# Kernel tuning notes

Measured on AMD Instinct MI355X. Metric: run time of the kernel, lower is better.

Reference implementation:

```python
import jax, jax.numpy as jnp
import numpy as np
from jax import lax

STRIDE = 16
ANCHOR_BASE = 16
PRE_NMS = 6000
POST_NMS = 2000
NMS_THRESH = 0.7


def _generate_anchors(base_size=16, ratios=(0.5, 1.0, 2.0), scales=(8, 16, 32)):
    w = h = float(base_size)
    x_ctr = 0.5 * (w - 1)
    y_ctr = 0.5 * (h - 1)
    size = w * h
    anchors = []
    for r in ratios:
        ws = np.round(np.sqrt(size / r))
        hs = np.round(ws * r)
        for s in scales:
            wss, hss = ws * s, hs * s
            anchors.append([x_ctr - 0.5 * (wss - 1), y_ctr - 0.5 * (hss - 1),
                            x_ctr + 0.5 * (wss - 1), y_ctr + 0.5 * (hss - 1)])
    return np.array(anchors, dtype=np.float32)  # [9,4]


def _all_anchors(width, height, stride):
    base = _generate_anchors(ANCHOR_BASE)  # [A,4]
    sx = np.arange(width, dtype=np.float32) * stride
    gy, gx = np.meshgrid(np.arange(height, dtype=np.float32) * stride, sx, indexing='ij')
    shifts = np.stack([gx.ravel(), gy.ravel(), gx.ravel(), gy.ravel()], axis=1)  # [K,4] h-major
    return jnp.asarray((shifts[:, None, :] + base[None, :, :]).reshape(-1, 4))  # [K*A,4]


def setup_inputs() -> dict:
    key = jax.random.key(0)
    k1, k2 = jax.random.split(key)
    H = W = 64
    bbox_deltas = jax.random.normal(k1, (1, 36, H, W), dtype=jnp.float32)
    scores = jax.random.uniform(k2, (1, 2, 9 * H, W), dtype=jnp.float32)
    return {"bbox_deltas": bbox_deltas, "scores": scores, "im_w": 1024, "im_h": 1024}


def reference(bbox_deltas, scores, im_w, im_h):
    H, W = bbox_deltas.shape[2], bbox_deltas.shape[3]
    # fg scores: reshape [1,2,9H,W] -> [1,18,H,W], take channels 9:18
    sc = scores.reshape(1, 18, H, W)[:, 9:, :, :].transpose(0, 2, 3, 1).reshape(-1)
    dl = bbox_deltas.transpose(0, 2, 3, 1).reshape(-1, 4)
    anchors = _all_anchors(W, H, STRIDE)

    # bbox_transform_inv (decode)
    aw = anchors[:, 2] - anchors[:, 0] + 1.0
    ah = anchors[:, 3] - anchors[:, 1] + 1.0
    acx = anchors[:, 0] + 0.5 * aw
    acy = anchors[:, 1] + 0.5 * ah
    pcx = dl[:, 0] * aw + acx
    pcy = dl[:, 1] * ah + acy
    pw = jnp.exp(dl[:, 2]) * aw
    ph = jnp.exp(dl[:, 3]) * ah
    x1 = jnp.clip(pcx - 0.5 * pw, 0.0, im_w - 1.0)
    y1 = jnp.clip(pcy - 0.5 * ph, 0.0, im_h - 1.0)
    x2 = jnp.clip(pcx + 0.5 * pw, 0.0, im_w - 1.0)
    y2 = jnp.clip(pcy + 0.5 * ph, 0.0, im_h - 1.0)
    props = jnp.stack([x1, y1, x2, y2], axis=1)

    # min-size filter
    thresh = 16.0 * (float(im_h) / float(im_w))
    keep_f = ((x2 - x1 + 1.0) >= thresh) & ((y2 - y1 + 1.0) >= thresh)
    sc_m = jnp.where(keep_f, sc, -jnp.inf)

    # pre-NMS top-k by score
    top_sc, idx = lax.top_k(sc_m, PRE_NMS)
    top_p = props[idx]  # [PRE_NMS,4], sorted by score desc
    valid = jnp.isfinite(top_sc)

    # pairwise IoU (with +1 box convention, as in py_cpu_nms)
    bx1, by1, bx2, by2 = top_p[:, 0], top_p[:, 1], top_p[:, 2], top_p[:, 3]
    areas = (bx2 - bx1 + 1.0) * (by2 - by1 + 1.0)
    iw = jnp.maximum(jnp.minimum(bx2[:, None], bx2[None, :]) - jnp.maximum(bx1[:, None], bx1[None, :]) + 1.0, 0.0)
    ih = jnp.maximum(jnp.minimum(by2[:, None], by2[None, :]) - jnp.maximum(by1[:, None], by1[None, :]) + 1.0, 0.0)
    inter = iw * ih
    iou = inter / (areas[:, None] + areas[None, :] - inter)
    sup = iou > NMS_THRESH  # [N,N]

    ar = jnp.arange(PRE_NMS)

    def body(i, keep):
        row = sup[i] & keep[i] & (ar > i)
        return keep & (~row)

    keep = lax.fori_loop(0, PRE_NMS, body, valid)

    # take first POST_NMS kept (in score order), scatter into fixed-size output
    rank = jnp.cumsum(keep.astype(jnp.int32)) - 1
    sel = keep & (rank < POST_NMS)
    dst = jnp.where(sel, rank, POST_NMS)  # invalid rows dumped into slot POST_NMS
    out_b = jnp.zeros((POST_NMS + 1, 4), dtype=jnp.float32).at[dst].set(
        jnp.where(sel[:, None], top_p, 0.0))[:POST_NMS]
    out_s = jnp.zeros((POST_NMS + 1,), dtype=jnp.float32).at[dst].set(
        jnp.where(sel, top_sc, 0.0))[:POST_NMS]
    blob = jnp.concatenate([jnp.zeros((POST_NMS, 1), dtype=jnp.float32), out_b], axis=1)
    return blob, out_s[:, None]
```

## Files before the change

kernel.cpp:

```cpp
#include <hip/hip_runtime.h>
#include <math.h>

typedef unsigned int u32;
typedef unsigned long long u64;

#define NANCH   36864
#define PRE     6000
#define POST    2000
#define NWORDS  94

#define OFF_PROPS   ((size_t)0)
#define OFF_SV      ((size_t)589824)
#define OFF_SORTED  ((size_t)884736)
#define OFF_SEL     ((size_t)932864)
#define OFF_MASK    ((size_t)1227776)
#define OFF_CTRL    ((size_t)5739776)
#define OFF_H1      ((size_t)5740032)
#define OFF_INVALW  ((size_t)5744384)
#define OFF_KEEPW   ((size_t)5745152)
#define ZERO_BYTES  ((size_t)(256 + 4352 + 768))

__device__ __constant__ float BA[9][4] = {
  {-84.f,-40.f,99.f,55.f},   {-176.f,-88.f,191.f,103.f}, {-360.f,-184.f,375.f,199.f},
  {-56.f,-56.f,71.f,71.f},   {-120.f,-120.f,135.f,135.f},{-248.f,-248.f,263.f,263.f},
  {-36.f,-80.f,51.f,95.f},   {-80.f,-168.f,95.f,183.f},  {-168.f,-344.f,183.f,359.f}};

__device__ __forceinline__ u32 key_bin(u32 key) {
  if (key < 0xBF000000u) return 0u;
  u32 b = ((key >> 13) - 0x5F800u) + 1u;
  return b > 1024u ? 1024u : b;
}

__global__ void decode_k(const float* __restrict__ deltas, const float* __restrict__ scores,
                         const int* __restrict__ imw_p, const int* __restrict__ imh_p,
                         float4* __restrict__ props, u64* __restrict__ sortvals,
                         u32* __restrict__ h1) {
  #pragma clang fp contract(off)
  int i = blockIdx.x * 256 + threadIdx.x;
  if (i >= NANCH) return;
  int a = i % 9;
  int pix = i / 9;
  int x = pix & 63, y = pix >> 6;

  float sc = scores[(9 + a) * 4096 + pix];
  float d0 = deltas[(a * 4 + 0) * 4096 + pix];
  float d1 = deltas[(a * 4 + 1) * 4096 + pix];
  float d2 = deltas[(a * 4 + 2) * 4096 + pix];
  float d3 = deltas[(a * 4 + 3) * 4096 + pix];

  float gx = (float)(x * 16), gy = (float)(y * 16);
  float ax1 = gx + BA[a][0], ay1 = gy + BA[a][1];
  float ax2 = gx + BA[a][2], ay2 = gy + BA[a][3];
  float aw = ax2 - ax1 + 1.0f, ah = ay2 - ay1 + 1.0f;
  float acx = ax1 + 0.5f * aw, acy = ay1 + 0.5f * ah;

  float pcx = d0 * aw + acx;
  float pcy = d1 * ah + acy;
  float pw = (float)exp((double)d2) * aw;
  float ph = (float)exp((double)d3) * ah;

  float imw1 = (float)imw_p[0] - 1.0f, imh1 = (float)imh_p[0] - 1.0f;
  float x1 = fminf(fmaxf(pcx - 0.5f * pw, 0.0f), imw1);
  float y1 = fminf(fmaxf(pcy - 0.5f * ph, 0.0f), imh1);
  float x2 = fminf(fmaxf(pcx + 0.5f * pw, 0.0f), imw1);
  float y2 = fminf(fmaxf(pcy + 0.5f * ph, 0.0f), imh1);
  props[i] = make_float4(x1, y1, x2, y2);

  float thresh = 16.0f * ((float)imh_p[0] / (float)imw_p[0]);
  bool keep = (x2 - x1 + 1.0f >= thresh) && (y2 - y1 + 1.0f >= thresh);
  u32 key = keep ? (__float_as_uint(sc) | 0x80000000u) : 0u;
  sortvals[i] = ((u64)key << 32) | (u64)(0xFFFFFFFFu - (u32)i);
  u32 bin = key_bin(key);
  if (bin) atomicAdd(&h1[bin], 1u);
}

__global__ void scan_k(const u32* __restrict__ h1, u32* __restrict__ ctrl) {
  int l = threadIdx.x;
  u32 loc[16], suf[16];
  #pragma unroll
  for (int k = 0; k < 16; ++k) loc[k] = h1[1 + l * 16 + k];
  u32 acc = 0;
  #pragma unroll
  for (int k = 15; k >= 0; --k) { acc += loc[k]; suf[k] = acc; }
  u32 sfx = acc;
  for (int off = 1; off < 64; off <<= 1) {
    u32 o = __shfl_down(sfx, off);
    if (l + off < 64) sfx += o;
  }
  u32 S_above = sfx - acc;
  u64 mball = __ballot(suf[0] + S_above >= (u32)PRE);
  if (mball == 0ULL) { if (l == 0) ctrl[0] = 0u; return; }
  int L = 63 - __builtin_clzll(mball);
  if (l == L) {
    int kk = 0;
    for (int k = 15; k >= 0; --k)
      if (suf[k] + S_above >= (u32)PRE) { kk = k; break; }
    ctrl[0] = (u32)(1 + 16 * L + kk);
  }
}

__global__ void compact_k(const u64* __restrict__ sv, u32* __restrict__ ctrl,
                          u64* __restrict__ sel) {
  int i = blockIdx.x * 256 + threadIdx.x;
  if (i >= NANCH) return;
  u32 chosen = ctrl[0];
  u64 v = sv[i];
  if (key_bin((u32)(v >> 32)) >= chosen) {
    u32 p = atomicAdd(&ctrl[6], 1u);
    sel[p] = v;
  }
}

__global__ void rank_k(const u64* __restrict__ sel, const u32* __restrict__ ctrl,
                       u64* __restrict__ sorted, u64* __restrict__ invalw) {
  __shared__ u64 sj[256];
  u32 n = ctrl[6];
  int i = blockIdx.x * 256 + threadIdx.x;
  if ((u32)(blockIdx.x * 256) >= n) return;
  u64 vi = ((u32)i < n) ? sel[i] : 0ULL;
  u32 cnt = 0;
  for (u32 jb = 0; jb < n; jb += 256) {
    __syncthreads();
    if (jb + threadIdx.x < n) sj[threadIdx.x] = sel[jb + threadIdx.x];
    __syncthreads();
    u32 m = min(256u, n - jb);
    #pragma unroll 8
    for (u32 j = 0; j < m; ++j) cnt += (u32)(sj[j] > vi);
  }
  if ((u32)i < n && cnt < (u32)PRE) {
    sorted[cnt] = vi;
    if ((u32)(vi >> 32) == 0u)
      atomicOr((unsigned long long*)&invalw[cnt >> 6], 1ULL << (cnt & 63));
  }
}

__global__ void mask_k(const u64* __restrict__ sorted, const float4* __restrict__ props,
                       u64* __restrict__ mask) {
  #pragma clang fp contract(off)
  __shared__ float4 cb[64];
  int jb = blockIdx.x;
  if (jb < (int)blockIdx.y) return;
  int i = blockIdx.y * 64 + threadIdx.x;
  int jj = jb * 64 + threadIdx.x;
  float4 cc = make_float4(0.f, 0.f, 0.f, 0.f);
  if (jj < PRE) {
    u64 v = sorted[jj];
    cc = props[0xFFFFu - ((u32)v & 0xFFFFu)];
  }
  cb[threadIdx.x] = cc;
  __syncthreads();
  if (i >= PRE) return;
  u64 vi = sorted[i];
  float4 b = props[0xFFFFu - ((u32)vi & 0xFFFFu)];
  float ai = (b.z - b.x + 1.0f) * (b.w - b.y + 1.0f);
  u64 bits = 0ULL;
  int jmax = min(64, PRE - jb * 64);
  for (int j = 0; j < jmax; ++j) {
    float4 c = cb[j];
    float aj = (c.z - c.x + 1.0f) * (c.w - c.y + 1.0f);
    float iw = fmaxf(fminf(b.z, c.z) - fmaxf(b.x, c.x) + 1.0f, 0.0f);
    float ih = fmaxf(fminf(b.w, c.w) - fmaxf(b.y, c.y) + 1.0f, 0.0f);
    float inter = iw * ih;
    float iou = inter / (ai + aj - inter);
    bits |= ((u64)(iou > 0.7f)) << j;
  }
  mask[(size_t)i * NWORDS + jb] = bits;
}

__device__ __forceinline__ void barrier_nodrain() {
  __builtin_amdgcn_sched_barrier(0);
  asm volatile("s_waitcnt lgkmcnt(0)" ::: "memory");
  __builtin_amdgcn_s_barrier();
  __builtin_amdgcn_sched_barrier(0);
}

__device__ __forceinline__ u64 rl64(u64 v, int lane) {
  u32 lo = (u32)__builtin_amdgcn_readlane((int)(u32)v, lane);
  u32 hi = (u32)__builtin_amdgcn_readlane((int)(u32)(v >> 32), lane);
  return ((u64)hi << 32) | (u64)lo;
}
__device__ __forceinline__ u64 rfl64(u64 v) {
  u32 lo = (u32)__builtin_amdgcn_readfirstlane((int)(u32)v);
  u32 hi = (u32)__builtin_amdgcn_readfirstlane((int)(u32)(v >> 32));
  return ((u64)hi << 32) | (u64)lo;
}

__global__ void __launch_bounds__(1024) nms_scan_k(const u64* __restrict__ mask,
                                                   const u64* __restrict__ invalw,
                                                   u64* __restrict__ keepw) {
  __shared__ u64 Lrem[NWORDS];
  __shared__ u64 Ldiag[64];
  __shared__ u64 Lkeep;
  __shared__ int Lstop;
  __shared__ int Llast;
  const int t = threadIdx.x;
  const int g = t >> 7;
  const int w = t & 127;
  const bool loader = (w < NWORDS);
  if (t < NWORDS) Lrem[t] = invalw[t];
  if (t == 0) { Lstop = 0; Llast = NWORDS - 1; }
  u64 rv = 0;
  u64 B0[8], B1[8], B2[8];
  int kept = 0;
  __syncthreads();

#define ISSUE(bb, BUF) \
  if ((bb) < NWORDS && loader) { \
    u64 st_ = Lrem[(bb)]; \
    const int row0_ = (bb) * 64 + g * 8; \
    const u64* pp_ = mask + (size_t)row0_ * NWORDS + w; \
    _Pragma("unroll") \
    for (int j = 0; j < 8; ++j) { \
      bool ok_ = (w >= (bb)) && (row0_ + j < PRE) && !((st_ >> (g * 8 + j)) & 1ULL); \
      BUF[j] = ok_ ? pp_[(size_t)j * NWORDS] : 0ULL; \
    } \
  }

#define STEP(bb, BUF) { \
    if (w == (bb)) {                      \
      atomicOr((u32*)&Lrem[(bb)], (u32)rv); \
      atomicOr(((u32*)&Lrem[(bb)]) + 1, (u32)(rv >> 32)); \
      _Pragma("unroll") \
      for (int j = 0; j < 8; ++j) Ldiag[g * 8 + j] = BUF[j]; \
    } \
    if ((bb) + 3 < NWORDS && w == (bb) + 3) {   \
      atomicOr((u32*)&Lrem[(bb) + 3], (u32)rv); \
      atomicOr(((u32*)&Lrem[(bb) + 3]) + 1, (u32)(rv >> 32)); \
    } \
    barrier_nodrain();                    \
    if (t < 64) { \
      u64 dgl = Ldiag[t]; \
      u64 avail = ~rfl64(Lrem[(bb)]);     \
      u64 kb = 0; \
      while (avail) { \
        int i_ = __builtin_ctzll(avail); \
        kb |= 1ULL << i_; \
        u64 di_ = rl64(dgl, i_); \
        avail &= ~di_ & ~((2ULL << i_) - 1ULL);  \
      } \
      if (t == 0) { \
        keepw[(bb)] = kb; \
        Lkeep = kb; \
        kept += (int)__popcll(kb); \
        if (kept >= POST) { Lstop = 1; Llast = (bb); } \
      } \
    } \
    barrier_nodrain();                    \
    { \
      u64 kb_ = Lkeep; \
      const int base_ = g * 8; \
      _Pragma("unroll") \
      for (int j = 0; j < 8; ++j) { \
        u64 k_ = (kb_ >> (base_ + j)) & 1ULL; \
        rv |= (0ULL - k_) & BUF[j]; \
      } \
    } \
    ISSUE((bb) + 3, BUF)                  \
    if (Lstop) break; }

  ISSUE(0, B0)
  ISSUE(1, B1)
  ISSUE(2, B2)
  for (int bb = 0; bb < NWORDS; bb += 3) {
    STEP(bb, B0)
    if (bb + 1 < NWORDS) STEP(bb + 1, B1)
    if (bb + 2 < NWORDS) STEP(bb + 2, B2)
  }
#undef ISSUE
#undef STEP

  __syncthreads();
  int last = Llast;
  for (int w2 = t; w2 < NWORDS; w2 += 1024)
    if (w2 > last) keepw[w2] = 0ULL;
}

__global__ void outscatter_k(const u64* __restrict__ keepw, const u64* __restrict__ sorted,
                             const float4* __restrict__ props, float* __restrict__ out) {
  __shared__ u64 wl[NWORDS];
  __shared__ u32 pre[NWORDS];
  int t = threadIdx.x;
  for (int i = t; i < 12000; i += 1024) out[i] = 0.0f;
  if (t < NWORDS) wl[t] = keepw[t];
  __syncthreads();
  if (t == 0) {
    u32 run = 0;
    for (int w = 0; w < NWORDS; ++w) { pre[w] = run; run += (u32)__popcll(wl[w]); }
  }
  __syncthreads();
  for (int i = t; i < PRE; i += 1024) {
    int w = i >> 6;
    u64 word = wl[w];
    if ((word >> (i & 63)) & 1ULL) {
      u32 rank = pre[w] + (u32)__popcll(word & ((1ULL << (i & 63)) - 1ULL));
      if (rank < POST) {
        u64 v = sorted[i];
        float4 b = props[0xFFFFu - ((u32)v & 0xFFFFu)];
        out[rank * 5 + 1] = b.x;
        out[rank * 5 + 2] = b.y;
        out[rank * 5 + 3] = b.z;
        out[rank * 5 + 4] = b.w;
        out[10000 + rank] = __uint_as_float((u32)(v >> 32) & 0x7FFFFFFFu);
      }
    }
  }
}

extern "C" void kernel_launch(void* const* d_in, const int* in_sizes, int n_in,
                              void* d_out, int out_size, void* d_ws, size_t ws_size,
                              hipStream_t stream) {
  const float* deltas = (const float*)d_in[0];
  const float* scores = (const float*)d_in[1];
  const int* imw = (const int*)d_in[2];
  const int* imh = (const int*)d_in[3];
  char* ws = (char*)d_ws;

  float4* props   = (float4*)(ws + OFF_PROPS);
  u64*    svals   = (u64*)(ws + OFF_SV);
  u64*    sorted  = (u64*)(ws + OFF_SORTED);
  u64*    sel     = (u64*)(ws + OFF_SEL);
  u64*    maskb   = (u64*)(ws + OFF_MASK);
  u32*    ctrl    = (u32*)(ws + OFF_CTRL);
  u32*    h1      = (u32*)(ws + OFF_H1);
  u64*    invalw  = (u64*)(ws + OFF_INVALW);
  u64*    keepw   = (u64*)(ws + OFF_KEEPW);

  hipMemsetAsync(ws + OFF_CTRL, 0, ZERO_BYTES, stream);

  decode_k<<<144, 256, 0, stream>>>(deltas, scores, imw, imh, props, svals, h1);
  scan_k<<<1, 64, 0, stream>>>(h1, ctrl);
  compact_k<<<144, 256, 0, stream>>>(svals, ctrl, sel);
  rank_k<<<144, 256, 0, stream>>>(sel, ctrl, sorted, invalw);

  dim3 mgrid(NWORDS, NWORDS);
  mask_k<<<mgrid, 64, 0, stream>>>(sorted, props, maskb);

  nms_scan_k<<<1, 1024, 0, stream>>>(maskb, invalw, keepw);
  outscatter_k<<<1, 1024, 0, stream>>>(keepw, sorted, props, (float*)d_out);
}
```

Measured before the change: 334.0 us.

## Fuse all proposal stages into one cooperative persistent kernel with grid syncs

Replaces the memset and seven separate launches (decode, histogram scan, compaction, rank sort, IoU mask, NMS scan, output scatter) with a single cooperative kernel of 256 blocks of 1024 threads. Stages are separated by grid-wide barriers. The IoU mask tiles are now spread over waves in a grid-stride loop instead of a 2D grid. The aim is to remove per-launch overhead and inter-kernel gaps. In exchange, the kernel relies on all blocks being co-resident and pays for several grid.sync barriers, and the serial NMS scan runs in one block while the others sit idle.

```diff
diff --git a/kernel.cpp b/kernel.cpp
--- a/kernel.cpp
+++ b/kernel.cpp
@@ -1,5 +1,8 @@
 #include <hip/hip_runtime.h>
+#include <hip/hip_cooperative_groups.h>
 #include <math.h>
+
+namespace cg = cooperative_groups;
 
 typedef unsigned int u32;
 typedef unsigned long long u64;
@@ -8,6 +11,8 @@
 #define PRE     6000
 #define POST    2000
 #define NWORDS  94
+#define NBLK    256
+#define TPB     1024
 
 #define OFF_PROPS   ((size_t)0)
 #define OFF_SV      ((size_t)589824)
@@ -18,7 +23,6 @@
 #define OFF_H1      ((size_t)5740032)
 #define OFF_INVALW  ((size_t)5744384)
 #define OFF_KEEPW   ((size_t)5745152)
-#define ZERO_BYTES  ((size_t)(256 + 4352 + 768))
 
 __device__ __constant__ float BA[9][4] = {
   {-84.f,-40.f,99.f,55.f},   {-176.f,-88.f,191.f,103.f}, {-360.f,-184.f,375.f,199.f},
@@ -29,142 +33,6 @@
   if (key < 0xBF000000u) return 0u;
   u32 b = ((key >> 13) - 0x5F800u) + 1u;
   return b > 1024u ? 1024u : b;
-}
-
-__global__ void decode_k(const float* __restrict__ deltas, const float* __restrict__ scores,
-                         const int* __restrict__ imw_p, const int* __restrict__ imh_p,
-                         float4* __restrict__ props, u64* __restrict__ sortvals,
-                         u32* __restrict__ h1) {
-  #pragma clang fp contract(off)
-  int i = blockIdx.x * 256 + threadIdx.x;
-  if (i >= NANCH) return;
-  int a = i % 9;
-  int pix = i / 9;
-  int x = pix & 63, y = pix >> 6;
-
-  float sc = scores[(9 + a) * 4096 + pix];
-  float d0 = deltas[(a * 4 + 0) * 4096 + pix];
-  float d1 = deltas[(a * 4 + 1) * 4096 + pix];
-  float d2 = deltas[(a * 4 + 2) * 4096 + pix];
-  float d3 = deltas[(a * 4 + 3) * 4096 + pix];
-
-  float gx = (float)(x * 16), gy = (float)(y * 16);
-  float ax1 = gx + BA[a][0], ay1 = gy + BA[a][1];
-  float ax2 = gx + BA[a][2], ay2 = gy + BA[a][3];
-  float aw = ax2 - ax1 + 1.0f, ah = ay2 - ay1 + 1.0f;
-  float acx = ax1 + 0.5f * aw, acy = ay1 + 0.5f * ah;
-
-  float pcx = d0 * aw + acx;
-  float pcy = d1 * ah + acy;
-  float pw = (float)exp((double)d2) * aw;
-  float ph = (float)exp((double)d3) * ah;
-
-  float imw1 = (float)imw_p[0] - 1.0f, imh1 = (float)imh_p[0] - 1.0f;
-  float x1 = fminf(fmaxf(pcx - 0.5f * pw, 0.0f), imw1);
-  float y1 = fminf(fmaxf(pcy - 0.5f * ph, 0.0f), imh1);
-  float x2 = fminf(fmaxf(pcx + 0.5f * pw, 0.0f), imw1);
-  float y2 = fminf(fmaxf(pcy + 0.5f * ph, 0.0f), imh1);
-  props[i] = make_float4(x1, y1, x2, y2);
-
-  float thresh = 16.0f * ((float)imh_p[0] / (float)imw_p[0]);
-  bool keep = (x2 - x1 + 1.0f >= thresh) && (y2 - y1 + 1.0f >= thresh);
-  u32 key = keep ? (__float_as_uint(sc) | 0x80000000u) : 0u;
-  sortvals[i] = ((u64)key << 32) | (u64)(0xFFFFFFFFu - (u32)i);
-  u32 bin = key_bin(key);
-  if (bin) atomicAdd(&h1[bin], 1u);
-}
-
-__global__ void scan_k(const u32* __restrict__ h1, u32* __restrict__ ctrl) {
-  int l = threadIdx.x;
-  u32 loc[16], suf[16];
-  #pragma unroll
-  for (int k = 0; k < 16; ++k) loc[k] = h1[1 + l * 16 + k];
-  u32 acc = 0;
-  #pragma unroll
-  for (int k = 15; k >= 0; --k) { acc += loc[k]; suf[k] = acc; }
-  u32 sfx = acc;
-  for (int off = 1; off < 64; off <<= 1) {
-    u32 o = __shfl_down(sfx, off);
-    if (l + off < 64) sfx += o;
-  }
-  u32 S_above = sfx - acc;
-  u64 mball = __ballot(suf[0] + S_above >= (u32)PRE);
-  if (mball == 0ULL) { if (l == 0) ctrl[0] = 0u; return; }
-  int L = 63 - __builtin_clzll(mball);
-  if (l == L) {
-    int kk = 0;
-    for (int k = 15; k >= 0; --k)
-      if (suf[k] + S_above >= (u32)PRE) { kk = k; break; }
-    ctrl[0] = (u32)(1 + 16 * L + kk);
-  }
-}
-
-__global__ void compact_k(const u64* __restrict__ sv, u32* __restrict__ ctrl,
-                          u64* __restrict__ sel) {
-  int i = blockIdx.x * 256 + threadIdx.x;
-  if (i >= NANCH) return;
-  u32 chosen = ctrl[0];
-  u64 v = sv[i];
-  if (key_bin((u32)(v >> 32)) >= chosen) {
-    u32 p = atomicAdd(&ctrl[6], 1u);
-    sel[p] = v;
-  }
-}
-
-__global__ void rank_k(const u64* __restrict__ sel, const u32* __restrict__ ctrl,
-                       u64* __restrict__ sorted, u64* __restrict__ invalw) {
-  __shared__ u64 sj[256];
-  u32 n = ctrl[6];
-  int i = blockIdx.x * 256 + threadIdx.x;
-  if ((u32)(blockIdx.x * 256) >= n) return;
-  u64 vi = ((u32)i < n) ? sel[i] : 0ULL;
-  u32 cnt = 0;
-  for (u32 jb = 0; jb < n; jb += 256) {
-    __syncthreads();
-    if (jb + threadIdx.x < n) sj[threadIdx.x] = sel[jb + threadIdx.x];
-    __syncthreads();
-    u32 m = min(256u, n - jb);
-    #pragma unroll 8
-    for (u32 j = 0; j < m; ++j) cnt += (u32)(sj[j] > vi);
-  }
-  if ((u32)i < n && cnt < (u32)PRE) {
-    sorted[cnt] = vi;
-    if ((u32)(vi >> 32) == 0u)
-      atomicOr((unsigned long long*)&invalw[cnt >> 6], 1ULL << (cnt & 63));
-  }
-}
-
-__global__ void mask_k(const u64* __restrict__ sorted, const float4* __restrict__ props,
-                       u64* __restrict__ mask) {
-  #pragma clang fp contract(off)
-  __shared__ float4 cb[64];
-  int jb = blockIdx.x;
-  if (jb < (int)blockIdx.y) return;
-  int i = blockIdx.y * 64 + threadIdx.x;
-  int jj = jb * 64 + threadIdx.x;
-  float4 cc = make_float4(0.f, 0.f, 0.f, 0.f);
-  if (jj < PRE) {
-    u64 v = sorted[jj];
-    cc = props[0xFFFFu - ((u32)v & 0xFFFFu)];
-  }
-  cb[threadIdx.x] = cc;
-  __syncthreads();
-  if (i >= PRE) return;
-  u64 vi = sorted[i];
-  float4 b = props[0xFFFFu - ((u32)vi & 0xFFFFu)];
-  float ai = (b.z - b.x + 1.0f) * (b.w - b.y + 1.0f);
-  u64 bits = 0ULL;
-  int jmax = min(64, PRE - jb * 64);
-  for (int j = 0; j < jmax; ++j) {
-    float4 c = cb[j];
-    float aj = (c.z - c.x + 1.0f) * (c.w - c.y + 1.0f);
-    float iw = fmaxf(fminf(b.z, c.z) - fmaxf(b.x, c.x) + 1.0f, 0.0f);
-    float ih = fmaxf(fminf(b.w, c.w) - fmaxf(b.y, c.y) + 1.0f, 0.0f);
-    float inter = iw * ih;
-    float iou = inter / (ai + aj - inter);
-    bits |= ((u64)(iou > 0.7f)) << j;
-  }
-  mask[(size_t)i * NWORDS + jb] = bits;
 }
 
 __device__ __forceinline__ void barrier_nodrain() {
@@ -185,30 +53,190 @@
   return ((u64)hi << 32) | (u64)lo;
 }
 
-__global__ void __launch_bounds__(1024) nms_scan_k(const u64* __restrict__ mask,
-                                                   const u64* __restrict__ invalw,
-                                                   u64* __restrict__ keepw) {
+__global__ void __launch_bounds__(TPB) fused_k(
+    const float* __restrict__ deltas, const float* __restrict__ scores,
+    const int* __restrict__ imw_p, const int* __restrict__ imh_p,
+    float4* __restrict__ props, u64* __restrict__ sorted,
+    u64* __restrict__ sel, u64* __restrict__ maskb,
+    u32* __restrict__ ctrl, u32* __restrict__ h1,
+    u64* __restrict__ invalw, u64* __restrict__ keepw,
+    float* __restrict__ out) {
+  #pragma clang fp contract(off)
+  cg::grid_group grid = cg::this_grid();
+  const int t = threadIdx.x;
+  const int b = blockIdx.x;
+  const int gtid = b * TPB + t;
+
+  __shared__ u64 sj[TPB];
+  __shared__ float4 cbm[16][64];
   __shared__ u64 Lrem[NWORDS];
   __shared__ u64 Ldiag[64];
   __shared__ u64 Lkeep;
   __shared__ int Lstop;
   __shared__ int Llast;
-  const int t = threadIdx.x;
-  const int g = t >> 7;
-  const int w = t & 127;
-  const bool loader = (w < NWORDS);
-  if (t < NWORDS) Lrem[t] = invalw[t];
-  if (t == 0) { Lstop = 0; Llast = NWORDS - 1; }
-  u64 rv = 0;
-  u64 B0[8], B1[8], B2[8];
-  int kept = 0;
-  __syncthreads();
+  __shared__ u32 prew[NWORDS];
+
+  u64 v = 0; u32 bin = 0; bool have = false;
+  if (gtid < NANCH) {
+    int a = gtid % 9;
+    int pix = gtid / 9;
+    int x = pix & 63, y = pix >> 6;
+
+    float sc = scores[(9 + a) * 4096 + pix];
+    float d0 = deltas[(a * 4 + 0) * 4096 + pix];
+    float d1 = deltas[(a * 4 + 1) * 4096 + pix];
+    float d2 = deltas[(a * 4 + 2) * 4096 + pix];
+    float d3 = deltas[(a * 4 + 3) * 4096 + pix];
+
+    float gx = (float)(x * 16), gy = (float)(y * 16);
+    float ax1 = gx + BA[a][0], ay1 = gy + BA[a][1];
+    float ax2 = gx + BA[a][2], ay2 = gy + BA[a][3];
+    float aw = ax2 - ax1 + 1.0f, ah = ay2 - ay1 + 1.0f;
+    float acx = ax1 + 0.5f * aw, acy = ay1 + 0.5f * ah;
+
+    float pcx = d0 * aw + acx;
+    float pcy = d1 * ah + acy;
+    float pw = (float)exp((double)d2) * aw;
+    float ph = (float)exp((double)d3) * ah;
+
+    float imw1 = (float)imw_p[0] - 1.0f, imh1 = (float)imh_p[0] - 1.0f;
+    float x1 = fminf(fmaxf(pcx - 0.5f * pw, 0.0f), imw1);
+    float y1 = fminf(fmaxf(pcy - 0.5f * ph, 0.0f), imh1);
+    float x2 = fminf(fmaxf(pcx + 0.5f * pw, 0.0f), imw1);
+    float y2 = fminf(fmaxf(pcy + 0.5f * ph, 0.0f), imh1);
+    props[gtid] = make_float4(x1, y1, x2, y2);
+
+    float thresh = 16.0f * ((float)imh_p[0] / (float)imw_p[0]);
+    bool keep = (x2 - x1 + 1.0f >= thresh) && (y2 - y1 + 1.0f >= thresh);
+    u32 key = keep ? (__float_as_uint(sc) | 0x80000000u) : 0u;
+    v = ((u64)key << 32) | (u64)(0xFFFFFFFFu - (u32)gtid);
+    bin = key_bin(key);
+    have = true;
+  }
+  if (b == 0) {
+    h1[t] = 0u;
+    if (t == 0) h1[1024] = 0u;
+    if (t < 64) ctrl[t] = 0u;
+    if (t < NWORDS) invalw[t] = 0ULL;
+  }
+  grid.sync();
+
+  if (have && bin) atomicAdd(&h1[bin], 1u);
+  grid.sync();
+
+  if (b == 0 && t < 64) {
+    int l = t;
+    u32 loc[16], suf[16];
+    #pragma unroll
+    for (int k = 0; k < 16; ++k) loc[k] = h1[1 + l * 16 + k];
+    u32 acc = 0;
+    #pragma unroll
+    for (int k = 15; k >= 0; --k) { acc += loc[k]; suf[k] = acc; }
+    u32 sfx = acc;
+    for (int off = 1; off < 64; off <<= 1) {
+      u32 o = __shfl_down(sfx, off);
+      if (l + off < 64) sfx += o;
+    }
+    u32 S_above = sfx - acc;
+    u64 mball = __ballot(suf[0] + S_above >= (u32)PRE);
+    if (mball == 0ULL) {
+      if (l == 0) ctrl[0] = 0u;
+    } else {
+      int L = 63 - __builtin_clzll(mball);
+      if (l == L) {
+        int kk = 0;
+        for (int k = 15; k >= 0; --k)
+          if (suf[k] + S_above >= (u32)PRE) { kk = k; break; }
+        ctrl[0] = (u32)(1 + 16 * L + kk);
+      }
+    }
+  }
+  grid.sync();
+
+  {
+    u32 chosen = ctrl[0];
+    if (have && key_bin((u32)(v >> 32)) >= chosen) {
+      u32 p = atomicAdd(&ctrl[6], 1u);
+      sel[p] = v;
+    }
+  }
+  grid.sync();
+
+  u32 n = ctrl[6];
+  if ((u32)(b * TPB) < n) {
+    u64 vi = ((u32)gtid < n) ? sel[gtid] : 0ULL;
+    u32 cnt = 0;
+    for (u32 jb = 0; jb < n; jb += TPB) {
+      __syncthreads();
+      if (jb + (u32)t < n) sj[t] = sel[jb + t];
+      __syncthreads();
+      u32 m = min((u32)TPB, n - jb);
+      #pragma unroll 8
+      for (u32 j = 0; j < m; ++j) cnt += (u32)(sj[j] > vi);
+    }
+    if ((u32)gtid < n && cnt < (u32)PRE) {
+      sorted[cnt] = vi;
+      if ((u32)(vi >> 32) == 0u)
+        atomicOr((unsigned long long*)&invalw[cnt >> 6], 1ULL << (cnt & 63));
+    }
+  }
+  grid.sync();
+
+  {
+    const int wv = t >> 6, lane = t & 63;
+    const int gw = b * 16 + wv;
+    for (int tile = gw; tile < NWORDS * NWORDS; tile += NBLK * 16) {
+      const int by = tile / NWORDS;
+      const int jb = tile - by * NWORDS;
+      if (jb < by) continue;
+      const int jj = jb * 64 + lane;
+      float4 cc = make_float4(0.f, 0.f, 0.f, 0.f);
+      if (jj < PRE) {
+        u64 vv = sorted[jj];
+        cc = props[0xFFFFu - ((u32)vv & 0xFFFFu)];
+      }
+      cbm[wv][lane] = cc;
+      __builtin_amdgcn_sched_barrier(0);
+      asm volatile("s_waitcnt lgkmcnt(0)" ::: "memory");
+      __builtin_amdgcn_sched_barrier(0);
+      const int i = by * 64 + lane;
+      if (i < PRE) {
+        u64 vi2 = sorted[i];
+        float4 bb = props[0xFFFFu - ((u32)vi2 & 0xFFFFu)];
+        float ai = (bb.z - bb.x + 1.0f) * (bb.w - bb.y + 1.0f);
+        u64 bits = 0ULL;
+        int jmax = min(64, PRE - jb * 64);
+        for (int j = 0; j < jmax; ++j) {
+          float4 c = cbm[wv][j];
+          float aj = (c.z - c.x + 1.0f) * (c.w - c.y + 1.0f);
+          float iw = fmaxf(fminf(bb.z, c.z) - fmaxf(bb.x, c.x) + 1.0f, 0.0f);
+          float ih = fmaxf(fminf(bb.w, c.w) - fmaxf(bb.y, c.y) + 1.0f, 0.0f);
+          float inter = iw * ih;
+          float iou = inter / (ai + aj - inter);
+          bits |= ((u64)(iou > 0.7f)) << j;
+        }
+        maskb[(size_t)i * NWORDS + jb] = bits;
+      }
+    }
+  }
+  grid.sync();
+
+  if (b == 0) {
+    const int g = t >> 7;
+    const int w = t & 127;
+    const bool loader = (w < NWORDS);
+    if (t < NWORDS) Lrem[t] = invalw[t];
+    if (t == 0) { Lstop = 0; Llast = NWORDS - 1; }
+    u64 rv = 0;
+    u64 B0[8], B1[8], B2[8];
+    int kept = 0;
+    __syncthreads();
 
 #define ISSUE(bb, BUF) \
   if ((bb) < NWORDS && loader) { \
     u64 st_ = Lrem[(bb)]; \
     const int row0_ = (bb) * 64 + g * 8; \
-    const u64* pp_ = mask + (size_t)row0_ * NWORDS + w; \
+    const u64* pp_ = maskb + (size_t)row0_ * NWORDS + w; \
     _Pragma("unroll") \
     for (int j = 0; j < 8; ++j) { \
       bool ok_ = (w >= (bb)) && (row0_ + j < PRE) && !((st_ >> (g * 8 + j)) & 1ULL); \
@@ -217,26 +245,26 @@
   }
 
 #define STEP(bb, BUF) { \
-    if (w == (bb)) {                      \
+    if (w == (bb)) { \
       atomicOr((u32*)&Lrem[(bb)], (u32)rv); \
       atomicOr(((u32*)&Lrem[(bb)]) + 1, (u32)(rv >> 32)); \
       _Pragma("unroll") \
       for (int j = 0; j < 8; ++j) Ldiag[g * 8 + j] = BUF[j]; \
     } \
-    if ((bb) + 3 < NWORDS && w == (bb) + 3) {   \
+    if ((bb) + 3 < NWORDS && w == (bb) + 3) { \
       atomicOr((u32*)&Lrem[(bb) + 3], (u32)rv); \
       atomicOr(((u32*)&Lrem[(bb) + 3]) + 1, (u32)(rv >> 32)); \
     } \
-    barrier_nodrain();                    \
+    barrier_nodrain(); \
     if (t < 64) { \
       u64 dgl = Ldiag[t]; \
-      u64 avail = ~rfl64(Lrem[(bb)]);     \
+      u64 avail = ~rfl64(Lrem[(bb)]); \
       u64 kb = 0; \
       while (avail) { \
         int i_ = __builtin_ctzll(avail); \
         kb |= 1ULL << i_; \
         u64 di_ = rl64(dgl, i_); \
-        avail &= ~di_ & ~((2ULL << i_) - 1ULL);  \
+        avail &= ~di_ & ~((2ULL << i_) - 1ULL); \
       } \
       if (t == 0) { \
         keepw[(bb)] = kb; \
@@ -245,7 +273,7 @@
         if (kept >= POST) { Lstop = 1; Llast = (bb); } \
       } \
     } \
-    barrier_nodrain();                    \
+    barrier_nodrain(); \
     { \
       u64 kb_ = Lkeep; \
       const int base_ = g * 8; \
@@ -255,52 +283,51 @@
         rv |= (0ULL - k_) & BUF[j]; \
       } \
     } \
-    ISSUE((bb) + 3, BUF)                  \
+    ISSUE((bb) + 3, BUF) \
     if (Lstop) break; }
 
-  ISSUE(0, B0)
-  ISSUE(1, B1)
-  ISSUE(2, B2)
-  for (int bb = 0; bb < NWORDS; bb += 3) {
-    STEP(bb, B0)
-    if (bb + 1 < NWORDS) STEP(bb + 1, B1)
-    if (bb + 2 < NWORDS) STEP(bb + 2, B2)
-  }
+    ISSUE(0, B0)
+    ISSUE(1, B1)
+    ISSUE(2, B2)
+    for (int bb = 0; bb < NWORDS; bb += 3) {
+      STEP(bb, B0)
+      if (bb + 1 < NWORDS) STEP(bb + 1, B1)
+      if (bb + 2 < NWORDS) STEP(bb + 2, B2)
+    }
 #undef ISSUE
 #undef STEP
 
-  __syncthreads();
-  int last = Llast;
-  for (int w2 = t; w2 < NWORDS; w2 += 1024)
-    if (w2 > last) keepw[w2] = 0ULL;
-}
-
-__global__ void outscatter_k(const u64* __restrict__ keepw, const u64* __restrict__ sorted,
-                             const float4* __restrict__ props, float* __restrict__ out) {
-  __shared__ u64 wl[NWORDS];
-  __shared__ u32 pre[NWORDS];
-  int t = threadIdx.x;
-  for (int i = t; i < 12000; i += 1024) out[i] = 0.0f;
-  if (t < NWORDS) wl[t] = keepw[t];
-  __syncthreads();
-  if (t == 0) {
-    u32 run = 0;
-    for (int w = 0; w < NWORDS; ++w) { pre[w] = run; run += (u32)__popcll(wl[w]); }
-  }
-  __syncthreads();
-  for (int i = t; i < PRE; i += 1024) {
-    int w = i >> 6;
-    u64 word = wl[w];
-    if ((word >> (i & 63)) & 1ULL) {
-      u32 rank = pre[w] + (u32)__popcll(word & ((1ULL << (i & 63)) - 1ULL));
-      if (rank < POST) {
-        u64 v = sorted[i];
-        float4 b = props[0xFFFFu - ((u32)v & 0xFFFFu)];
-        out[rank * 5 + 1] = b.x;
-        out[rank * 5 + 2] = b.y;
-        out[rank * 5 + 3] = b.z;
-        out[rank * 5 + 4] = b.w;
-        out[10000 + rank] = __uint_as_float((u32)(v >> 32) & 0x7FFFFFFFu);
+    __syncthreads();
+    int last = Llast;
+    for (int w2 = t; w2 < NWORDS; w2 += TPB)
+      if (w2 > last) keepw[w2] = 0ULL;
+  } else {
+    for (int i = (b - 1) * TPB + t; i < 12000; i += (NBLK - 1) * TPB) out[i] = 0.0f;
+  }
+  grid.sync();
+
+  if (b == 0) {
+    if (t < NWORDS) Lrem[t] = keepw[t];
+    __syncthreads();
+    if (t == 0) {
+      u32 run = 0;
+      for (int w2 = 0; w2 < NWORDS; ++w2) { prew[w2] = run; run += (u32)__popcll(Lrem[w2]); }
+    }
+    __syncthreads();
+    for (int i = t; i < PRE; i += TPB) {
+      int w2 = i >> 6;
+      u64 word = Lrem[w2];
+      if ((word >> (i & 63)) & 1ULL) {
+        u32 rank = prew[w2] + (u32)__popcll(word & ((1ULL << (i & 63)) - 1ULL));
+        if (rank < POST) {
+          u64 vv = sorted[i];
+          float4 bx = props[0xFFFFu - ((u32)vv & 0xFFFFu)];
+          out[rank * 5 + 1] = bx.x;
+          out[rank * 5 + 2] = bx.y;
+          out[rank * 5 + 3] = bx.z;
+          out[rank * 5 + 4] = bx.w;
+          out[10000 + rank] = __uint_as_float((u32)(vv >> 32) & 0x7FFFFFFFu);
+        }
       }
     }
   }
@@ -316,7 +343,6 @@
   char* ws = (char*)d_ws;
 
   float4* props   = (float4*)(ws + OFF_PROPS);
-  u64*    svals   = (u64*)(ws + OFF_SV);
   u64*    sorted  = (u64*)(ws + OFF_SORTED);
   u64*    sel     = (u64*)(ws + OFF_SEL);
   u64*    maskb   = (u64*)(ws + OFF_MASK);
@@ -324,17 +350,11 @@
   u32*    h1      = (u32*)(ws + OFF_H1);
   u64*    invalw  = (u64*)(ws + OFF_INVALW);
   u64*    keepw   = (u64*)(ws + OFF_KEEPW);
-
-  hipMemsetAsync(ws + OFF_CTRL, 0, ZERO_BYTES, stream);
-
-  decode_k<<<144, 256, 0, stream>>>(deltas, scores, imw, imh, props, svals, h1);
-  scan_k<<<1, 64, 0, stream>>>(h1, ctrl);
-  compact_k<<<144, 256, 0, stream>>>(svals, ctrl, sel);
-  rank_k<<<144, 256, 0, stream>>>(sel, ctrl, sorted, invalw);
-
-  dim3 mgrid(NWORDS, NWORDS);
-  mask_k<<<mgrid, 64, 0, stream>>>(sorted, props, maskb);
-
-  nms_scan_k<<<1, 1024, 0, stream>>>(maskb, invalw, keepw);
-  outscatter_k<<<1, 1024, 0, stream>>>(keepw, sorted, props, (float*)d_out);
-}
+  float*  outp    = (float*)d_out;
+
+  void* kargs[] = { (void*)&deltas, (void*)&scores, (void*)&imw, (void*)&imh,
+                    (void*)&props, (void*)&sorted, (void*)&sel, (void*)&maskb,
+                    (void*)&ctrl, (void*)&h1, (void*)&invalw, (void*)&keepw,
+                    (void*)&outp };
+  hipLaunchCooperativeKernel((void*)fused_k, dim3(NBLK), dim3(TPB), kargs, 0, stream);
+}
```

Measured after the change: 525.4 us. +57.3%, slower.

## Restructure NMS scan to one barrier per word with wave-specialized diagonal resolver

Applied to the files above, without the earlier changes.

The sequential NMS scan drops from two block barriers per 64-row word to one. A dedicated first wave resolves each diagonal block. It keeps the diagonal and off-diagonal mask tiles in registers, prefetches them one step ahead, and folds the previous word's kept-row suppression into the current word with a butterfly shuffle OR-reduction. The remaining waves accumulate suppression one step late through a double-buffered keep word, using two register buffers instead of three. This cuts synchronization on the serial critical path, at the cost of extra shuffles, global loads on the resolver wave, and subtler cross-step dependency logic.

```diff
diff --git a/kernel.cpp b/kernel.cpp
--- a/kernel.cpp
+++ b/kernel.cpp
@@ -184,24 +184,34 @@
   u32 hi = (u32)__builtin_amdgcn_readfirstlane((int)(u32)(v >> 32));
   return ((u64)hi << 32) | (u64)lo;
 }
+__device__ __forceinline__ u64 sx64(u64 v, int m) {
+  u32 lo = (u32)__shfl_xor((int)(u32)v, m);
+  u32 hi = (u32)__shfl_xor((int)(u32)(v >> 32), m);
+  return ((u64)hi << 32) | (u64)lo;
+}
 
 __global__ void __launch_bounds__(1024) nms_scan_k(const u64* __restrict__ mask,
                                                    const u64* __restrict__ invalw,
                                                    u64* __restrict__ keepw) {
   __shared__ u64 Lrem[NWORDS];
-  __shared__ u64 Ldiag[64];
-  __shared__ u64 Lkeep;
+  __shared__ u64 LkeepBuf[2];
   __shared__ int Lstop;
   __shared__ int Llast;
   const int t = threadIdx.x;
-  const int g = t >> 7;
-  const int w = t & 127;
-  const bool loader = (w < NWORDS);
+  const int tl = t - 64;
+  const bool inL = (tl >= 0 && tl < 768);
+  const int w = inL ? (tl % 96) : 127;
+  const int g = inL ? (tl / 96) : 0;
+  const bool loader = inL && (w < NWORDS);
+
   if (t < NWORDS) Lrem[t] = invalw[t];
-  if (t == 0) { Lstop = 0; Llast = NWORDS - 1; }
+  if (t == 0) { Lstop = 0; Llast = NWORDS - 1; LkeepBuf[0] = 0ULL; LkeepBuf[1] = 0ULL; }
+
   u64 rv = 0;
-  u64 B0[8], B1[8], B2[8];
+  u64 B0[8], B1[8];
+  u64 Td = 0, Toff = 0, kbPrev = 0;
   int kept = 0;
+  if (t < 64) Td = mask[(size_t)t * NWORDS + 0];
   __syncthreads();
 
 #define ISSUE(bb, BUF) \
@@ -216,58 +226,60 @@
     } \
   }
 
-#define STEP(bb, BUF) { \
-    if (w == (bb)) {                      \
-      atomicOr((u32*)&Lrem[(bb)], (u32)rv); \
-      atomicOr(((u32*)&Lrem[(bb)]) + 1, (u32)(rv >> 32)); \
-      _Pragma("unroll") \
-      for (int j = 0; j < 8; ++j) Ldiag[g * 8 + j] = BUF[j]; \
-    } \
-    if ((bb) + 3 < NWORDS && w == (bb) + 3) {   \
-      atomicOr((u32*)&Lrem[(bb) + 3], (u32)rv); \
-      atomicOr(((u32*)&Lrem[(bb) + 3]) + 1, (u32)(rv >> 32)); \
-    } \
+#define STEPX(s, BUF) { \
     barrier_nodrain();                    \
+    if (Lstop) break; \
     if (t < 64) { \
-      u64 dgl = Ldiag[t]; \
-      u64 avail = ~rfl64(Lrem[(bb)]);     \
+      u64 c_ = ((kbPrev >> t) & 1ULL) ? Toff : 0ULL; \
+      c_ |= sx64(c_, 1);  c_ |= sx64(c_, 2);  c_ |= sx64(c_, 4); \
+      c_ |= sx64(c_, 8);  c_ |= sx64(c_, 16); c_ |= sx64(c_, 32); \
+      u64 avail = ~(rfl64(Lrem[(s)]) | c_); \
       u64 kb = 0; \
       while (avail) { \
         int i_ = __builtin_ctzll(avail); \
         kb |= 1ULL << i_; \
-        u64 di_ = rl64(dgl, i_); \
+        u64 di_ = rl64(Td, i_); \
         avail &= ~di_ & ~((2ULL << i_) - 1ULL);  \
       } \
+      u64 TdN = 0, ToffN = 0; \
+      if ((s) + 1 < NWORDS) {             \
+        int rN_ = ((s) + 1) * 64 + t; \
+        if (rN_ < PRE) TdN = mask[(size_t)rN_ * NWORDS + ((s) + 1)]; \
+        ToffN = mask[(size_t)((s) * 64 + t) * NWORDS + ((s) + 1)]; \
+      } \
       if (t == 0) { \
-        keepw[(bb)] = kb; \
-        Lkeep = kb; \
+        keepw[(s)] = kb; \
+        LkeepBuf[(s) & 1] = kb; \
         kept += (int)__popcll(kb); \
-        if (kept >= POST) { Lstop = 1; Llast = (bb); } \
+        if (kept >= POST) { Lstop = 1; Llast = (s); } \
       } \
+      kbPrev = kb; Td = TdN; Toff = ToffN; \
     } \
-    barrier_nodrain();                    \
-    { \
-      u64 kb_ = Lkeep; \
-      const int base_ = g * 8; \
-      _Pragma("unroll") \
-      for (int j = 0; j < 8; ++j) { \
-        u64 k_ = (kb_ >> (base_ + j)) & 1ULL; \
-        rv |= (0ULL - k_) & BUF[j]; \
+    if (loader) { \
+      if ((s) >= 1) { \
+        u64 kp_ = LkeepBuf[((s) - 1) & 1];    \
+        const int base_ = g * 8; \
+        _Pragma("unroll") \
+        for (int j = 0; j < 8; ++j) { \
+          u64 k_ = (kp_ >> (base_ + j)) & 1ULL; \
+          rv |= (0ULL - k_) & BUF[j]; \
+        } \
+        if (w == (s) + 1) {               \
+          atomicOr((u32*)&Lrem[(s) + 1], (u32)rv); \
+          atomicOr(((u32*)&Lrem[(s) + 1]) + 1, (u32)(rv >> 32)); \
+        } \
       } \
+      ISSUE((s) + 1, BUF)                 \
     } \
-    ISSUE((bb) + 3, BUF)                  \
-    if (Lstop) break; }
+  }
 
   ISSUE(0, B0)
-  ISSUE(1, B1)
-  ISSUE(2, B2)
-  for (int bb = 0; bb < NWORDS; bb += 3) {
-    STEP(bb, B0)
-    if (bb + 1 < NWORDS) STEP(bb + 1, B1)
-    if (bb + 2 < NWORDS) STEP(bb + 2, B2)
+  for (int s = 0; s < NWORDS; s += 2) {
+    STEPX(s, B1)
+    if (s + 1 < NWORDS) STEPX(s + 1, B0)
   }
 #undef ISSUE
-#undef STEP
+#undef STEPX
 
   __syncthreads();
   int last = Llast;
```

Result: no change. 338.7 us (+1.4%).
